# Kernel tuning notes

Measured on AMD Instinct MI355X. Metric: run time of the kernel, lower is better.

Reference implementation:

```python
import math
import jax, jax.numpy as jnp
import numpy as np

D_MODEL = 512
NUM_HEADS = 8
D_TRACK = 64
EPS = 1e-6


def setup_inputs() -> dict:
    key = jax.random.key(0)
    ks = jax.random.split(key, 8)
    B, C, T = 2, 4096, 16
    lecun = lambda k, shp: jax.random.normal(k, shp, jnp.float32) / jnp.sqrt(jnp.float32(shp[0]))
    return {
        "x": jax.random.normal(ks[0], (B, C, D_MODEL), jnp.float32),
        "track_embeddings": jax.random.normal(ks[1], (B, T, C, D_TRACK), jnp.float32),
        "norm_scale": jnp.ones((D_MODEL,), jnp.float32),
        "wq": lecun(ks[2], (D_MODEL, D_MODEL)), "bq": jnp.zeros((D_MODEL,), jnp.float32),
        "wk": lecun(ks[3], (D_TRACK, D_MODEL)), "bk": jnp.zeros((D_MODEL,), jnp.float32),
        "wv": lecun(ks[4], (D_TRACK, D_MODEL)), "bv": jnp.zeros((D_MODEL,), jnp.float32),
        "wo": lecun(ks[5], (D_MODEL, D_MODEL)), "bo": jnp.zeros((D_MODEL,), jnp.float32),
    }


def reference(x, track_embeddings, norm_scale, wq, bq, wk, bk, wv, bv, wo, bo):
    B, C, D = x.shape
    T = track_embeddings.shape[1]
    H = NUM_HEADS
    d_head = D // H
    residual = x
    # RMSNorm
    xn = x * jax.lax.rsqrt(jnp.mean(jnp.square(x), axis=-1, keepdims=True) + EPS) * norm_scale
    Q = (xn @ wq + bq).reshape(B, C, H, d_head)
    track_flat = track_embeddings.transpose(0, 2, 1, 3)  # (B, C, T, d_track)
    K = (track_flat @ wk + bk).reshape(B, C, T, H, d_head)
    V = (track_flat @ wv + bv).reshape(B, C, T, H, d_head)
    scale = 1.0 / math.sqrt(d_head)
    attn_logits = jnp.einsum('bchd,bcthd->bcht', Q, K) * scale
    attn_weights = jax.nn.softmax(attn_logits, axis=-1)
    attn_out = jnp.einsum('bcht,bcthd->bchd', attn_weights, V).reshape(B, C, D)
    return residual + attn_out @ wo + bo
```

## Files before the change

kernel.cpp:

```cpp
#include <hip/hip_runtime.h>
#include <math.h>


#define NTOK 8192

typedef __attribute__((ext_vector_type(8))) short short8;
typedef __attribute__((ext_vector_type(8))) unsigned short ushort8;
typedef __attribute__((ext_vector_type(4))) unsigned short ushort4v;
typedef __attribute__((ext_vector_type(4))) float f32x4;

__device__ __forceinline__ unsigned short f2bf(float f) {
    unsigned int u = __float_as_uint(f);
    unsigned int r = (u + 0x7fffu + ((u >> 16) & 1u)) >> 16;
    return (unsigned short)r;
}
__device__ __forceinline__ float bf2f(unsigned short s) {
    return __uint_as_float(((unsigned int)s) << 16);
}

__device__ __forceinline__ void gl_lds16(const void* g, void* l) {
    __builtin_amdgcn_global_load_lds(
        (const __attribute__((address_space(1))) unsigned int*)g,
        (__attribute__((address_space(3))) unsigned int*)l,
        16, 0, 0);
}


__global__ __launch_bounds__(256) void kprep(
    const float* __restrict__ x, const float* __restrict__ nscale,
    const float* __restrict__ wq, const float* __restrict__ bq,
    const float* __restrict__ wk, const float* __restrict__ wv,
    const float* __restrict__ bv, const float* __restrict__ wo,
    const float* __restrict__ bo,
    unsigned short* __restrict__ wqkT, float* __restrict__ bqk,
    unsigned short* __restrict__ wvoT, float* __restrict__ bvo,
    unsigned short* __restrict__ xnb)
{
    const int bid = blockIdx.x;
    const int t = threadIdx.x;
    if (bid < 64) {
        __shared__ float wkL[64][65];
        __shared__ float wqL[64][65];
        const int h = bid >> 3;
        const int i0 = (bid & 7) * 64;
        #pragma unroll
        for (int i = 0; i < 16; ++i) {
            const int idx = t + i * 256;
            const int d = idx >> 6, e = idx & 63;
            wkL[d][e] = wk[(size_t)d * 512 + h * 64 + e];
            wqL[d][e] = wq[(size_t)(i0 + d) * 512 + h * 64 + e];
        }
        __syncthreads();
        const int d = t & 63, ig = t >> 6;
        float acc[16];
        #pragma unroll
        for (int ii = 0; ii < 16; ++ii) acc[ii] = 0.f;
        for (int e = 0; e < 64; ++e) {
            const float kv = wkL[d][e];
            #pragma unroll
            for (int ii = 0; ii < 16; ++ii)
                acc[ii] += kv * wqL[ig * 16 + ii][e];
        }
        #pragma unroll
        for (int ii = 0; ii < 16; ++ii)
            wqkT[(size_t)(h * 64 + d) * 512 + i0 + ig * 16 + ii] = f2bf(acc[ii]);
        if (((bid & 7) == 0) && ig == 0) {
            float a = 0.f;
            #pragma unroll
            for (int e = 0; e < 64; ++e) a += bq[h * 64 + e] * wkL[d][e];
            bqk[h * 64 + d] = a;
        }
    } else if (bid < 128) {
        __shared__ float wvL[64][65];
        __shared__ float woL[64][65];
        const int b2 = bid - 64;
        const int h = b2 >> 3;
        const int j0 = (b2 & 7) * 64;
        #pragma unroll
        for (int i = 0; i < 16; ++i) {
            const int idx = t + i * 256;
            const int a = idx >> 6, b = idx & 63;
            wvL[a][b] = wv[(size_t)a * 512 + h * 64 + b];
            woL[a][b] = wo[(size_t)(h * 64 + a) * 512 + j0 + b];
        }
        __syncthreads();
        const int jloc = t & 63, dg = t >> 6;
        float acc[16];
        #pragma unroll
        for (int dd = 0; dd < 16; ++dd) acc[dd] = 0.f;
        for (int e = 0; e < 64; ++e) {
            const float b = woL[e][jloc];
            #pragma unroll
            for (int dd = 0; dd < 16; ++dd)
                acc[dd] += wvL[dg * 16 + dd][e] * b;
        }
        #pragma unroll
        for (int dd = 0; dd < 16; ++dd)
            wvoT[(size_t)(j0 + jloc) * 512 + h * 64 + dg * 16 + dd] = f2bf(acc[dd]);
    } else if (bid < 192) {
        const int b3 = bid - 128;
        const int j = b3 * 8 + (t >> 5);
        const int l = t & 31;
        float p = 0.f;
        #pragma unroll 4
        for (int e = l; e < 512; e += 32) p += bv[e] * wo[(size_t)e * 512 + j];
        #pragma unroll
        for (int m = 1; m < 32; m <<= 1) p += __shfl_xor(p, m, 64);
        if (l == 0) bvo[j] = bo[j] + p;
    } else {
        const int row = (bid - 192) * 4 + (t >> 6);
        const int lane = t & 63;
        const float* xr = x + (size_t)row * 512 + lane * 8;
        const float4 v0 = *reinterpret_cast<const float4*>(xr);
        const float4 v1 = *reinterpret_cast<const float4*>(xr + 4);
        float s = v0.x*v0.x + v0.y*v0.y + v0.z*v0.z + v0.w*v0.w
                + v1.x*v1.x + v1.y*v1.y + v1.z*v1.z + v1.w*v1.w;
        #pragma unroll
        for (int m = 1; m < 64; m <<= 1) s += __shfl_xor(s, m, 64);
        const float r = rsqrtf(s * (1.f / 512.f) + 1e-6f);
        const float4 s0 = *reinterpret_cast<const float4*>(nscale + lane * 8);
        const float4 s1 = *reinterpret_cast<const float4*>(nscale + lane * 8 + 4);
        ushort8 o;
        o[0] = f2bf(v0.x * r * s0.x); o[1] = f2bf(v0.y * r * s0.y);
        o[2] = f2bf(v0.z * r * s0.z); o[3] = f2bf(v0.w * r * s0.w);
        o[4] = f2bf(v1.x * r * s1.x); o[5] = f2bf(v1.y * r * s1.y);
        o[6] = f2bf(v1.z * r * s1.z); o[7] = f2bf(v1.w * r * s1.w);
        *reinterpret_cast<ushort8*>(xnb + (size_t)row * 512 + lane * 8) = o;
    }
}


template<int MODE>
__global__ __launch_bounds__(256) void kG(
    const unsigned short* __restrict__ A,
    const unsigned short* __restrict__ Bt,
    const float* __restrict__ bias,
    const float* __restrict__ resid,
    void* __restrict__ outp)
{
    __shared__ __align__(16) unsigned short Asm[2][128 * 64];
    __shared__ __align__(16) unsigned short Bsm[2][64 * 64];
    const int tid = threadIdx.x;
    const int hw = blockIdx.x;
    const int logical = (hw & 7) * 64 + (hw >> 3);
    const int mt = logical >> 3, nt = logical & 7;
    const int tok0 = mt * 128, n0 = nt * 64;
    const int w = tid >> 6, lane = tid & 63;
    const int wr = w >> 1, wc = w & 1;
    const int lrow = lane & 15, lk = lane >> 4;

    float pb[2];
    float rr[2][4][4];
    #pragma unroll
    for (int n = 0; n < 2; ++n) {
        const int ocol = n0 + wc * 32 + n * 16 + lrow;
        pb[n] = bias[ocol];
        if (MODE == 1) {
            #pragma unroll
            for (int m = 0; m < 4; ++m)
                #pragma unroll
                for (int r = 0; r < 4; ++r) {
                    const int orow = tok0 + wr * 64 + m * 16 + lk * 4 + r;
                    rr[n][m][r] = resid[(size_t)orow * 512 + ocol];
                }
        }
    }

    const int srowA[4] = { (tid + 0) >> 3, (tid + 256) >> 3, (tid + 512) >> 3, (tid + 768) >> 3 };
    const int sc8 = tid & 7;

    auto STAGE = [&](int buf, int k0) {
        #pragma unroll
        for (int i = 0; i < 4; ++i) {
            const int f = tid + i * 256;
            const int row = srowA[i];
            const int c8s = sc8 ^ (row & 7);
            gl_lds16(A + (size_t)(tok0 + row) * 512 + k0 + c8s * 8,
                     (char*)&Asm[buf][0] + f * 16);
        }
        #pragma unroll
        for (int i = 0; i < 2; ++i) {
            const int f = tid + i * 256;
            const int row = f >> 3;
            const int c8s = sc8 ^ (row & 7);
            gl_lds16(Bt + (size_t)(n0 + row) * 512 + k0 + c8s * 8,
                     (char*)&Bsm[buf][0] + f * 16);
        }
    };

    f32x4 acc[4][2] = {};
    STAGE(0, 0);
    __syncthreads();
    for (int it = 0; it < 8; ++it) {
        const int cur = it & 1;
        if (it < 7) STAGE(cur ^ 1, (it + 1) * 64);
        #pragma unroll
        for (int kk = 0; kk < 2; ++kk) {
            short8 a[4], b[2];
            #pragma unroll
            for (int m = 0; m < 4; ++m) {
                const int r = wr * 64 + m * 16 + lrow;
                const int byte = (r * 128 + kk * 64 + lk * 16) ^ ((r & 7) << 4);
                a[m] = *reinterpret_cast<const short8*>((const char*)&Asm[cur][0] + byte);
            }
            #pragma unroll
            for (int n = 0; n < 2; ++n) {
                const int r = wc * 32 + n * 16 + lrow;
                const int byte = (r * 128 + kk * 64 + lk * 16) ^ ((r & 7) << 4);
                b[n] = *reinterpret_cast<const short8*>((const char*)&Bsm[cur][0] + byte);
            }
            #pragma unroll
            for (int m = 0; m < 4; ++m)
                #pragma unroll
                for (int n = 0; n < 2; ++n)
                    acc[m][n] = __builtin_amdgcn_mfma_f32_16x16x32_bf16(
                        a[m], b[n], acc[m][n], 0, 0, 0);
        }
        __syncthreads();
    }
    #pragma unroll
    for (int n = 0; n < 2; ++n) {
        const int ocol = n0 + wc * 32 + n * 16 + lrow;
        #pragma unroll
        for (int m = 0; m < 4; ++m) {
            #pragma unroll
            for (int r = 0; r < 4; ++r) {
                const int orow = tok0 + wr * 64 + m * 16 + lk * 4 + r;
                float v = acc[m][n][r] + pb[n];
                if (MODE == 0) {
                    ((unsigned short*)outp)[(size_t)orow * 512 + ocol] = f2bf(v);
                } else {
                    v += rr[n][m][r];
                    ((float*)outp)[(size_t)orow * 512 + ocol] = v;
                }
            }
        }
    }
}


__global__ __launch_bounds__(256) void k3_attn(
    const float* __restrict__ track, const unsigned short* __restrict__ qwb,
    unsigned short* __restrict__ wtfb)
{
    __shared__ __align__(16) float tf[2][16][68];
    __shared__ __align__(16) float qwl[2][8][68];
    __shared__ float lw[2][8][16];
    const int tid = threadIdx.x;
    const int tok = tid >> 7;
    const int t2 = tid & 127;
    const int token = blockIdx.x * 2 + tok;
    const int b = token >> 12;
    const int c = token & 4095;
    #pragma unroll
    for (int i = 0; i < 2; ++i) {
        const int f = t2 + i * 128;
        const int row = f >> 4, d4 = (f & 15) * 4;
        *reinterpret_cast<float4*>(&tf[tok][row][d4]) =
            *reinterpret_cast<const float4*>(track + ((size_t)(b * 16 + row) * 4096 + c) * 64 + d4);
    }
    if (t2 < 64) {
        const ushort8 q = *reinterpret_cast<const ushort8*>(qwb + (size_t)token * 512 + t2 * 8);
        #pragma unroll
        for (int j = 0; j < 8; ++j) {
            const int idx = t2 * 8 + j;
            qwl[tok][idx >> 6][idx & 63] = bf2f(q[j]);
        }
    }
    __syncthreads();
    {
        const int h = t2 >> 4, tt = t2 & 15;
        float acc = 0.f;
        #pragma unroll
        for (int d16 = 0; d16 < 16; ++d16) {
            const float4 qv = *reinterpret_cast<const float4*>(&qwl[tok][h][d16 * 4]);
            const float4 tv = *reinterpret_cast<const float4*>(&tf[tok][tt][d16 * 4]);
            acc += qv.x * tv.x + qv.y * tv.y + qv.z * tv.z + qv.w * tv.w;
        }
        float lg = acc * 0.125f;
        float mx = lg;
        #pragma unroll
        for (int m = 1; m < 16; m <<= 1) mx = fmaxf(mx, __shfl_xor(mx, m, 64));
        const float ev = __expf(lg - mx);
        float sum = ev;
        #pragma unroll
        for (int m = 1; m < 16; m <<= 1) sum += __shfl_xor(sum, m, 64);
        lw[tok][h][tt] = ev / sum;
    }
    __syncthreads();
    {
        const int h = t2 >> 4;
        const int d0 = (t2 & 15) * 4;
        float o0 = 0.f, o1 = 0.f, o2 = 0.f, o3 = 0.f;
        #pragma unroll
        for (int t = 0; t < 16; ++t) {
            const float wgt = lw[tok][h][t];
            const float4 tv = *reinterpret_cast<const float4*>(&tf[tok][t][d0]);
            o0 += wgt * tv.x; o1 += wgt * tv.y; o2 += wgt * tv.z; o3 += wgt * tv.w;
        }
        ushort4v ov;
        ov[0] = f2bf(o0); ov[1] = f2bf(o1); ov[2] = f2bf(o2); ov[3] = f2bf(o3);
        *reinterpret_cast<ushort4v*>(wtfb + (size_t)token * 512 + t2 * 4) = ov;
    }
}

extern "C" void kernel_launch(void* const* d_in, const int* in_sizes, int n_in,
                              void* d_out, int out_size, void* d_ws, size_t ws_size,
                              hipStream_t stream) {
    const float* x      = (const float*)d_in[0];
    const float* track  = (const float*)d_in[1];
    const float* nscale = (const float*)d_in[2];
    const float* wq     = (const float*)d_in[3];
    const float* bq     = (const float*)d_in[4];
    const float* wk     = (const float*)d_in[5];
    const float* wv     = (const float*)d_in[7];
    const float* bv     = (const float*)d_in[8];
    const float* wo     = (const float*)d_in[9];
    const float* bo     = (const float*)d_in[10];
    float* buf = (float*)d_out;

    char* ws = (char*)d_ws;
    unsigned short* xnb  = (unsigned short*)ws;
    unsigned short* qwb  = (unsigned short*)(ws + 8388608);
    unsigned short* wqkT = (unsigned short*)(ws + 16777216);
    unsigned short* wvoT = (unsigned short*)(ws + 17301504);
    float* bqk = (float*)(ws + 17825792);
    float* bvo = (float*)(ws + 17827840);

    kprep<<<192 + NTOK / 4, 256, 0, stream>>>(x, nscale, wq, bq, wk, wv, bv, wo, bo,
                                              wqkT, bqk, wvoT, bvo, xnb);
    kG<0><<<512, 256, 0, stream>>>(xnb, wqkT, bqk, nullptr, qwb);
    k3_attn<<<NTOK / 2, 256, 0, stream>>>(track, qwb, xnb);
    kG<1><<<512, 256, 0, stream>>>(xnb, wvoT, bvo, x, buf);
}
```

Baseline: 52.35 us.

## Fuse RMSNorm, Q·Wk projection and track attention into one kernel

Removes the separate RMSNorm pass and the bf16 xn/qw intermediates. The new kernel loads fp32 x directly, converts it to bf16 in LDS and accumulates the sum of squares on the fly. It folds norm_scale into the precomputed Wq·Wk weights and applies the rsqrt row scale after the MFMA GEMM. The per-head attention over the 16 track slots runs in the same block, staging the track data via async global-to-LDS loads. This cuts a kernel launch and several global round-trips. In exchange the attention phase now runs per 64-column head tile with 8 tokens per step, and track data is reloaded once per head tile.

Measured after the change: 79.81 us. 52.5% more time.

```diff
diff --git a/kernel.cpp b/kernel.cpp
--- a/kernel.cpp
+++ b/kernel.cpp
@@ -6,7 +6,7 @@
 
 typedef __attribute__((ext_vector_type(8))) short short8;
 typedef __attribute__((ext_vector_type(8))) unsigned short ushort8;
-typedef __attribute__((ext_vector_type(4))) unsigned short ushort4v;
+typedef __attribute__((ext_vector_type(2))) unsigned short ushort2v;
 typedef __attribute__((ext_vector_type(4))) float f32x4;
 
 __device__ __forceinline__ unsigned short f2bf(float f) {
@@ -17,7 +17,6 @@
 __device__ __forceinline__ float bf2f(unsigned short s) {
     return __uint_as_float(((unsigned int)s) << 16);
 }
-
 __device__ __forceinline__ void gl_lds16(const void* g, void* l) {
     __builtin_amdgcn_global_load_lds(
         (const __attribute__((address_space(1))) unsigned int*)g,
@@ -27,14 +26,12 @@
 
 
 __global__ __launch_bounds__(256) void kprep(
-    const float* __restrict__ x, const float* __restrict__ nscale,
     const float* __restrict__ wq, const float* __restrict__ bq,
     const float* __restrict__ wk, const float* __restrict__ wv,
     const float* __restrict__ bv, const float* __restrict__ wo,
-    const float* __restrict__ bo,
+    const float* __restrict__ bo, const float* __restrict__ nscale,
     unsigned short* __restrict__ wqkT, float* __restrict__ bqk,
-    unsigned short* __restrict__ wvoT, float* __restrict__ bvo,
-    unsigned short* __restrict__ xnb)
+    unsigned short* __restrict__ wvoT, float* __restrict__ bvo)
 {
     const int bid = blockIdx.x;
     const int t = threadIdx.x;
@@ -62,8 +59,10 @@
                 acc[ii] += kv * wqL[ig * 16 + ii][e];
         }
         #pragma unroll
-        for (int ii = 0; ii < 16; ++ii)
-            wqkT[(size_t)(h * 64 + d) * 512 + i0 + ig * 16 + ii] = f2bf(acc[ii]);
+        for (int ii = 0; ii < 16; ++ii) {
+            const int i = i0 + ig * 16 + ii;
+            wqkT[(size_t)(h * 64 + d) * 512 + i] = f2bf(acc[ii] * nscale[i]);
+        }
         if (((bid & 7) == 0) && ig == 0) {
             float a = 0.f;
             #pragma unroll
@@ -97,7 +96,7 @@
         #pragma unroll
         for (int dd = 0; dd < 16; ++dd)
             wvoT[(size_t)(j0 + jloc) * 512 + h * 64 + dg * 16 + dd] = f2bf(acc[dd]);
-    } else if (bid < 192) {
+    } else {
         const int b3 = bid - 128;
         const int j = b3 * 8 + (t >> 5);
         const int l = t & 31;
@@ -107,36 +106,195 @@
         #pragma unroll
         for (int m = 1; m < 32; m <<= 1) p += __shfl_xor(p, m, 64);
         if (l == 0) bvo[j] = bo[j] + p;
-    } else {
-        const int row = (bid - 192) * 4 + (t >> 6);
-        const int lane = t & 63;
-        const float* xr = x + (size_t)row * 512 + lane * 8;
-        const float4 v0 = *reinterpret_cast<const float4*>(xr);
-        const float4 v1 = *reinterpret_cast<const float4*>(xr + 4);
-        float s = v0.x*v0.x + v0.y*v0.y + v0.z*v0.z + v0.w*v0.w
-                + v1.x*v1.x + v1.y*v1.y + v1.z*v1.z + v1.w*v1.w;
-        #pragma unroll
-        for (int m = 1; m < 64; m <<= 1) s += __shfl_xor(s, m, 64);
-        const float r = rsqrtf(s * (1.f / 512.f) + 1e-6f);
-        const float4 s0 = *reinterpret_cast<const float4*>(nscale + lane * 8);
-        const float4 s1 = *reinterpret_cast<const float4*>(nscale + lane * 8 + 4);
-        ushort8 o;
-        o[0] = f2bf(v0.x * r * s0.x); o[1] = f2bf(v0.y * r * s0.y);
-        o[2] = f2bf(v0.z * r * s0.z); o[3] = f2bf(v0.w * r * s0.w);
-        o[4] = f2bf(v1.x * r * s1.x); o[5] = f2bf(v1.y * r * s1.y);
-        o[6] = f2bf(v1.z * r * s1.z); o[7] = f2bf(v1.w * r * s1.w);
-        *reinterpret_cast<ushort8*>(xnb + (size_t)row * 512 + lane * 8) = o;
-    }
-}
-
-
-template<int MODE>
-__global__ __launch_bounds__(256) void kG(
+    }
+}
+
+
+__global__ __launch_bounds__(256) void kF(
+    const float* __restrict__ x, const float* __restrict__ track,
+    const unsigned short* __restrict__ wqkT, const float* __restrict__ bqk,
+    unsigned short* __restrict__ wtfb)
+{
+    __shared__ __align__(16) char pool[81920];
+    const int tid = threadIdx.x;
+    const int hw = blockIdx.x;
+    const int logical = (hw & 7) * 64 + (hw >> 3);
+    const int mt = logical >> 3, nt = logical & 7;
+    const int tok0 = mt * 128, n0 = nt * 64;
+    const int w = tid >> 6, lane = tid & 63;
+    const int wr = w >> 1, wc = w & 1;
+    const int lrow = lane & 15, lk = lane >> 4;
+    float* rls = (float*)(pool + 49152);
+
+    float pb[2];
+    #pragma unroll
+    for (int n = 0; n < 2; ++n) pb[n] = bqk[n0 + wc * 32 + n * 16 + lrow];
+
+    const int arow = tid >> 1;
+    const int ac0 = (tid & 1) * 4;
+    const float* xrow = x + (size_t)(tok0 + arow) * 512 + ac0 * 8;
+
+    auto stageB = [&](int buf, int k0) {
+        #pragma unroll
+        for (int i = 0; i < 2; ++i) {
+            const int f = tid + i * 256;
+            const int row = f >> 3, c8 = f & 7;
+            const int c8s = c8 ^ (row & 7);
+            gl_lds16(wqkT + (size_t)(n0 + row) * 512 + k0 + c8s * 8,
+                     pool + 32768 + buf * 8192 + f * 16);
+        }
+    };
+
+    float ssq = 0.f;
+    float4 v[8];
+    auto packA = [&](int buf) {
+        #pragma unroll
+        for (int c2 = 0; c2 < 4; ++c2) {
+            const float4 a0 = v[c2 * 2], a1 = v[c2 * 2 + 1];
+            ssq += a0.x*a0.x + a0.y*a0.y + a0.z*a0.z + a0.w*a0.w
+                 + a1.x*a1.x + a1.y*a1.y + a1.z*a1.z + a1.w*a1.w;
+            ushort8 o;
+            o[0]=f2bf(a0.x); o[1]=f2bf(a0.y); o[2]=f2bf(a0.z); o[3]=f2bf(a0.w);
+            o[4]=f2bf(a1.x); o[5]=f2bf(a1.y); o[6]=f2bf(a1.z); o[7]=f2bf(a1.w);
+            *reinterpret_cast<ushort8*>(
+                pool + buf * 16384 + arow * 128 + (((ac0 + c2) ^ (arow & 7)) << 4)) = o;
+        }
+    };
+
+    #pragma unroll
+    for (int j = 0; j < 8; ++j) v[j] = *reinterpret_cast<const float4*>(xrow + j * 4);
+    stageB(0, 0);
+    packA(0);
+    __syncthreads();
+
+    f32x4 acc[4][2] = {};
+    for (int it = 0; it < 8; ++it) {
+        const int cur = it & 1;
+        if (it < 7) {
+            stageB(cur ^ 1, (it + 1) * 64);
+            #pragma unroll
+            for (int j = 0; j < 8; ++j)
+                v[j] = *reinterpret_cast<const float4*>(xrow + (it + 1) * 64 + j * 4);
+        }
+        #pragma unroll
+        for (int kk = 0; kk < 2; ++kk) {
+            short8 a[4], b[2];
+            #pragma unroll
+            for (int m = 0; m < 4; ++m) {
+                const int r = wr * 64 + m * 16 + lrow;
+                const int byte = (r * 128 + kk * 64 + lk * 16) ^ ((r & 7) << 4);
+                a[m] = *reinterpret_cast<const short8*>(pool + cur * 16384 + byte);
+            }
+            #pragma unroll
+            for (int n = 0; n < 2; ++n) {
+                const int rB = wc * 32 + n * 16 + lrow;
+                const int byte = (rB * 128 + kk * 64 + lk * 16) ^ ((rB & 7) << 4);
+                b[n] = *reinterpret_cast<const short8*>(pool + 32768 + cur * 8192 + byte);
+            }
+            #pragma unroll
+            for (int m = 0; m < 4; ++m)
+                #pragma unroll
+                for (int n = 0; n < 2; ++n)
+                    acc[m][n] = __builtin_amdgcn_mfma_f32_16x16x32_bf16(
+                        a[m], b[n], acc[m][n], 0, 0, 0);
+        }
+        if (it < 7) packA(cur ^ 1);
+        __syncthreads();
+    }
+
+    {
+        const float tot = ssq + __shfl_xor(ssq, 1, 64);
+        if ((tid & 1) == 0) rls[arow] = rsqrtf(tot * (1.f / 512.f) + 1e-6f);
+    }
+    __syncthreads();
+
+    auto stageTF = [&](int pbuf, int p) {
+        char* base = pool + 16384 + pbuf * 32768;
+        #pragma unroll
+        for (int i = 0; i < 8; ++i) {
+            const int f = tid + i * 256;
+            const int tl = f >> 8, t = (f >> 4) & 15, dc = f & 15;
+            const int token = tok0 + p * 8 + tl;
+            const int bb = token >> 12, cc = token & 4095;
+            const int dcs = dc ^ (t & 7);
+            gl_lds16(track + ((size_t)(bb * 16 + t) * 4096 + cc) * 64 + dcs * 4,
+                     base + f * 16);
+        }
+    };
+    stageTF(0, 0);
+
+    #pragma unroll
+    for (int n = 0; n < 2; ++n) {
+        const int col = wc * 32 + n * 16 + lrow;
+        #pragma unroll
+        for (int m = 0; m < 4; ++m) {
+            #pragma unroll
+            for (int r2 = 0; r2 < 4; ++r2) {
+                const int row = wr * 64 + m * 16 + lk * 4 + r2;
+                const float qv = acc[m][n][r2] * rls[row] + pb[n];
+                *reinterpret_cast<unsigned short*>(
+                    pool + row * 128 + (((col >> 3) ^ (row & 7)) << 4) + (col & 7) * 2) = f2bf(qv);
+            }
+        }
+    }
+    __syncthreads();
+
+    const int tl = tid >> 5;
+    const int sub = tid & 31;
+    const int tslot = sub & 15, half = sub >> 4;
+    const int dpv = sub * 2;
+    for (int p = 0; p < 16; ++p) {
+        if (p < 15) stageTF((p + 1) & 1, p + 1);
+        const char* TFb = pool + 16384 + (p & 1) * 32768;
+        const char* tokb = TFb + tl * 4096;
+        const int qrow = p * 8 + tl;
+        float qf[32];
+        #pragma unroll
+        for (int jq = 0; jq < 4; ++jq) {
+            const ushort8 qv = *reinterpret_cast<const ushort8*>(
+                pool + qrow * 128 + (((half * 4 + jq) ^ (qrow & 7)) << 4));
+            #pragma unroll
+            for (int e = 0; e < 8; ++e) qf[jq * 8 + e] = bf2f((unsigned short)qv[e]);
+        }
+        float acc1 = 0.f;
+        #pragma unroll
+        for (int jj = 0; jj < 8; ++jj) {
+            const float4 tv = *reinterpret_cast<const float4*>(
+                tokb + tslot * 256 + (((half * 8 + jj) ^ (tslot & 7)) << 4));
+            acc1 += qf[jj*4+0]*tv.x + qf[jj*4+1]*tv.y + qf[jj*4+2]*tv.z + qf[jj*4+3]*tv.w;
+        }
+        acc1 += __shfl_xor(acc1, 16, 64);
+        const float lg = acc1 * 0.125f;
+        float mx = lg;
+        #pragma unroll
+        for (int msk = 1; msk < 16; msk <<= 1) mx = fmaxf(mx, __shfl_xor(mx, msk, 64));
+        const float ev = __expf(lg - mx);
+        float sm = ev;
+        #pragma unroll
+        for (int msk = 1; msk < 16; msk <<= 1) sm += __shfl_xor(sm, msk, 64);
+        const float wgt = ev / sm;
+        float o0 = 0.f, o1 = 0.f;
+        #pragma unroll
+        for (int t = 0; t < 16; ++t) {
+            const float wt = __shfl(wgt, (lane & 48) + t, 64);
+            const float2 tv = *reinterpret_cast<const float2*>(
+                tokb + t * 256 + (((dpv >> 2) ^ (t & 7)) << 4) + (dpv & 3) * 4);
+            o0 += wt * tv.x; o1 += wt * tv.y;
+        }
+        ushort2v ow; ow[0] = f2bf(o0); ow[1] = f2bf(o1);
+        const int token = tok0 + p * 8 + tl;
+        *reinterpret_cast<ushort2v*>(wtfb + (size_t)token * 512 + n0 + dpv) = ow;
+        __syncthreads();
+    }
+}
+
+
+__global__ __launch_bounds__(256) void kG2(
     const unsigned short* __restrict__ A,
     const unsigned short* __restrict__ Bt,
     const float* __restrict__ bias,
     const float* __restrict__ resid,
-    void* __restrict__ outp)
+    float* __restrict__ out)
 {
     __shared__ __align__(16) unsigned short Asm[2][128 * 64];
     __shared__ __align__(16) unsigned short Bsm[2][64 * 64];
@@ -155,20 +313,17 @@
     for (int n = 0; n < 2; ++n) {
         const int ocol = n0 + wc * 32 + n * 16 + lrow;
         pb[n] = bias[ocol];
-        if (MODE == 1) {
-            #pragma unroll
-            for (int m = 0; m < 4; ++m)
-                #pragma unroll
-                for (int r = 0; r < 4; ++r) {
-                    const int orow = tok0 + wr * 64 + m * 16 + lk * 4 + r;
-                    rr[n][m][r] = resid[(size_t)orow * 512 + ocol];
-                }
-        }
+        #pragma unroll
+        for (int m = 0; m < 4; ++m)
+            #pragma unroll
+            for (int r = 0; r < 4; ++r) {
+                const int orow = tok0 + wr * 64 + m * 16 + lk * 4 + r;
+                rr[n][m][r] = resid[(size_t)orow * 512 + ocol];
+            }
     }
 
     const int srowA[4] = { (tid + 0) >> 3, (tid + 256) >> 3, (tid + 512) >> 3, (tid + 768) >> 3 };
     const int sc8 = tid & 7;
-
     auto STAGE = [&](int buf, int k0) {
         #pragma unroll
         for (int i = 0; i < 4; ++i) {
@@ -226,81 +381,9 @@
             #pragma unroll
             for (int r = 0; r < 4; ++r) {
                 const int orow = tok0 + wr * 64 + m * 16 + lk * 4 + r;
-                float v = acc[m][n][r] + pb[n];
-                if (MODE == 0) {
-                    ((unsigned short*)outp)[(size_t)orow * 512 + ocol] = f2bf(v);
-                } else {
-                    v += rr[n][m][r];
-                    ((float*)outp)[(size_t)orow * 512 + ocol] = v;
-                }
-            }
-        }
-    }
-}
-
-
-__global__ __launch_bounds__(256) void k3_attn(
-    const float* __restrict__ track, const unsigned short* __restrict__ qwb,
-    unsigned short* __restrict__ wtfb)
-{
-    __shared__ __align__(16) float tf[2][16][68];
-    __shared__ __align__(16) float qwl[2][8][68];
-    __shared__ float lw[2][8][16];
-    const int tid = threadIdx.x;
-    const int tok = tid >> 7;
-    const int t2 = tid & 127;
-    const int token = blockIdx.x * 2 + tok;
-    const int b = token >> 12;
-    const int c = token & 4095;
-    #pragma unroll
-    for (int i = 0; i < 2; ++i) {
-        const int f = t2 + i * 128;
-        const int row = f >> 4, d4 = (f & 15) * 4;
-        *reinterpret_cast<float4*>(&tf[tok][row][d4]) =
-            *reinterpret_cast<const float4*>(track + ((size_t)(b * 16 + row) * 4096 + c) * 64 + d4);
-    }
-    if (t2 < 64) {
-        const ushort8 q = *reinterpret_cast<const ushort8*>(qwb + (size_t)token * 512 + t2 * 8);
-        #pragma unroll
-        for (int j = 0; j < 8; ++j) {
-            const int idx = t2 * 8 + j;
-            qwl[tok][idx >> 6][idx & 63] = bf2f(q[j]);
-        }
-    }
-    __syncthreads();
-    {
-        const int h = t2 >> 4, tt = t2 & 15;
-        float acc = 0.f;
-        #pragma unroll
-        for (int d16 = 0; d16 < 16; ++d16) {
-            const float4 qv = *reinterpret_cast<const float4*>(&qwl[tok][h][d16 * 4]);
-            const float4 tv = *reinterpret_cast<const float4*>(&tf[tok][tt][d16 * 4]);
-            acc += qv.x * tv.x + qv.y * tv.y + qv.z * tv.z + qv.w * tv.w;
-        }
-        float lg = acc * 0.125f;
-        float mx = lg;
-        #pragma unroll
-        for (int m = 1; m < 16; m <<= 1) mx = fmaxf(mx, __shfl_xor(mx, m, 64));
-        const float ev = __expf(lg - mx);
-        float sum = ev;
-        #pragma unroll
-        for (int m = 1; m < 16; m <<= 1) sum += __shfl_xor(sum, m, 64);
-        lw[tok][h][tt] = ev / sum;
-    }
-    __syncthreads();
-    {
-        const int h = t2 >> 4;
-        const int d0 = (t2 & 15) * 4;
-        float o0 = 0.f, o1 = 0.f, o2 = 0.f, o3 = 0.f;
-        #pragma unroll
-        for (int t = 0; t < 16; ++t) {
-            const float wgt = lw[tok][h][t];
-            const float4 tv = *reinterpret_cast<const float4*>(&tf[tok][t][d0]);
-            o0 += wgt * tv.x; o1 += wgt * tv.y; o2 += wgt * tv.z; o3 += wgt * tv.w;
-        }
-        ushort4v ov;
-        ov[0] = f2bf(o0); ov[1] = f2bf(o1); ov[2] = f2bf(o2); ov[3] = f2bf(o3);
-        *reinterpret_cast<ushort4v*>(wtfb + (size_t)token * 512 + t2 * 4) = ov;
+                out[(size_t)orow * 512 + ocol] = acc[m][n][r] + pb[n] + rr[n][m][r];
+            }
+        }
     }
 }
 
@@ -320,16 +403,14 @@
     float* buf = (float*)d_out;
 
     char* ws = (char*)d_ws;
-    unsigned short* xnb  = (unsigned short*)ws;
-    unsigned short* qwb  = (unsigned short*)(ws + 8388608);
-    unsigned short* wqkT = (unsigned short*)(ws + 16777216);
-    unsigned short* wvoT = (unsigned short*)(ws + 17301504);
-    float* bqk = (float*)(ws + 17825792);
-    float* bvo = (float*)(ws + 17827840);
-
-    kprep<<<192 + NTOK / 4, 256, 0, stream>>>(x, nscale, wq, bq, wk, wv, bv, wo, bo,
-                                              wqkT, bqk, wvoT, bvo, xnb);
-    kG<0><<<512, 256, 0, stream>>>(xnb, wqkT, bqk, nullptr, qwb);
-    k3_attn<<<NTOK / 2, 256, 0, stream>>>(track, qwb, xnb);
-    kG<1><<<512, 256, 0, stream>>>(xnb, wvoT, bvo, x, buf);
-}
+    unsigned short* wtfb = (unsigned short*)ws;
+    unsigned short* wqkT = (unsigned short*)(ws + 8388608);
+    unsigned short* wvoT = (unsigned short*)(ws + 8912896);
+    float* bqk = (float*)(ws + 9437184);
+    float* bvo = (float*)(ws + 9439232);
+
+    kprep<<<192, 256, 0, stream>>>(wq, bq, wk, wv, bv, wo, bo, nscale,
+                                   wqkT, bqk, wvoT, bvo);
+    kF<<<512, 256, 0, stream>>>(x, track, wqkT, bqk, wtfb);
+    kG2<<<512, 256, 0, stream>>>(wtfb, wvoT, bvo, x, buf);
+}
```

## Fuse RMSNorm into the Q·Wk GEMM and fold norm scale into weights

Applied to the files above, without the earlier changes.

RMSNorm moves out of the prep kernel and into the first GEMM. The GEMM loads fp32 x directly, converts it to bf16 into LDS while accumulating per-row sums of squares, and applies the rsqrt row scale in the epilogue. The norm scale is folded into the precomputed Wq·Wk^T weights, and the 1/sqrt(d) factor moves from the attention kernel into the GEMM epilogue. This removes the bf16 normalized-x round trip through global memory, at the cost of register-staged A loads in place of direct global-to-LDS copies and twice the A-tile read bytes, since the input is now fp32.

Measured after the change: 61.64 us. 17.7% more time.

```diff
diff --git a/kernel.cpp b/kernel.cpp
--- a/kernel.cpp
+++ b/kernel.cpp
@@ -17,7 +17,6 @@
 __device__ __forceinline__ float bf2f(unsigned short s) {
     return __uint_as_float(((unsigned int)s) << 16);
 }
-
 __device__ __forceinline__ void gl_lds16(const void* g, void* l) {
     __builtin_amdgcn_global_load_lds(
         (const __attribute__((address_space(1))) unsigned int*)g,
@@ -27,14 +26,12 @@
 
 
 __global__ __launch_bounds__(256) void kprep(
-    const float* __restrict__ x, const float* __restrict__ nscale,
     const float* __restrict__ wq, const float* __restrict__ bq,
     const float* __restrict__ wk, const float* __restrict__ wv,
     const float* __restrict__ bv, const float* __restrict__ wo,
-    const float* __restrict__ bo,
+    const float* __restrict__ bo, const float* __restrict__ nscale,
     unsigned short* __restrict__ wqkT, float* __restrict__ bqk,
-    unsigned short* __restrict__ wvoT, float* __restrict__ bvo,
-    unsigned short* __restrict__ xnb)
+    unsigned short* __restrict__ wvoT, float* __restrict__ bvo)
 {
     const int bid = blockIdx.x;
     const int t = threadIdx.x;
@@ -62,8 +59,10 @@
                 acc[ii] += kv * wqL[ig * 16 + ii][e];
         }
         #pragma unroll
-        for (int ii = 0; ii < 16; ++ii)
-            wqkT[(size_t)(h * 64 + d) * 512 + i0 + ig * 16 + ii] = f2bf(acc[ii]);
+        for (int ii = 0; ii < 16; ++ii) {
+            const int i = i0 + ig * 16 + ii;
+            wqkT[(size_t)(h * 64 + d) * 512 + i] = f2bf(acc[ii] * nscale[i]);
+        }
         if (((bid & 7) == 0) && ig == 0) {
             float a = 0.f;
             #pragma unroll
@@ -97,7 +96,7 @@
         #pragma unroll
         for (int dd = 0; dd < 16; ++dd)
             wvoT[(size_t)(j0 + jloc) * 512 + h * 64 + dg * 16 + dd] = f2bf(acc[dd]);
-    } else if (bid < 192) {
+    } else {
         const int b3 = bid - 128;
         const int j = b3 * 8 + (t >> 5);
         const int l = t & 31;
@@ -107,39 +106,18 @@
         #pragma unroll
         for (int m = 1; m < 32; m <<= 1) p += __shfl_xor(p, m, 64);
         if (l == 0) bvo[j] = bo[j] + p;
-    } else {
-        const int row = (bid - 192) * 4 + (t >> 6);
-        const int lane = t & 63;
-        const float* xr = x + (size_t)row * 512 + lane * 8;
-        const float4 v0 = *reinterpret_cast<const float4*>(xr);
-        const float4 v1 = *reinterpret_cast<const float4*>(xr + 4);
-        float s = v0.x*v0.x + v0.y*v0.y + v0.z*v0.z + v0.w*v0.w
-                + v1.x*v1.x + v1.y*v1.y + v1.z*v1.z + v1.w*v1.w;
-        #pragma unroll
-        for (int m = 1; m < 64; m <<= 1) s += __shfl_xor(s, m, 64);
-        const float r = rsqrtf(s * (1.f / 512.f) + 1e-6f);
-        const float4 s0 = *reinterpret_cast<const float4*>(nscale + lane * 8);
-        const float4 s1 = *reinterpret_cast<const float4*>(nscale + lane * 8 + 4);
-        ushort8 o;
-        o[0] = f2bf(v0.x * r * s0.x); o[1] = f2bf(v0.y * r * s0.y);
-        o[2] = f2bf(v0.z * r * s0.z); o[3] = f2bf(v0.w * r * s0.w);
-        o[4] = f2bf(v1.x * r * s1.x); o[5] = f2bf(v1.y * r * s1.y);
-        o[6] = f2bf(v1.z * r * s1.z); o[7] = f2bf(v1.w * r * s1.w);
-        *reinterpret_cast<ushort8*>(xnb + (size_t)row * 512 + lane * 8) = o;
-    }
-}
-
-
-template<int MODE>
-__global__ __launch_bounds__(256) void kG(
-    const unsigned short* __restrict__ A,
-    const unsigned short* __restrict__ Bt,
-    const float* __restrict__ bias,
-    const float* __restrict__ resid,
-    void* __restrict__ outp)
+    }
+}
+
+
+__global__ __launch_bounds__(256) void kRG1(
+    const float* __restrict__ x,
+    const unsigned short* __restrict__ wqkT, const float* __restrict__ bqk,
+    unsigned short* __restrict__ qwb)
 {
     __shared__ __align__(16) unsigned short Asm[2][128 * 64];
     __shared__ __align__(16) unsigned short Bsm[2][64 * 64];
+    __shared__ float rls[128];
     const int tid = threadIdx.x;
     const int hw = blockIdx.x;
     const int logical = (hw & 7) * 64 + (hw >> 3);
@@ -150,50 +128,62 @@
     const int lrow = lane & 15, lk = lane >> 4;
 
     float pb[2];
-    float rr[2][4][4];
-    #pragma unroll
-    for (int n = 0; n < 2; ++n) {
-        const int ocol = n0 + wc * 32 + n * 16 + lrow;
-        pb[n] = bias[ocol];
-        if (MODE == 1) {
-            #pragma unroll
-            for (int m = 0; m < 4; ++m)
-                #pragma unroll
-                for (int r = 0; r < 4; ++r) {
-                    const int orow = tok0 + wr * 64 + m * 16 + lk * 4 + r;
-                    rr[n][m][r] = resid[(size_t)orow * 512 + ocol];
-                }
-        }
-    }
-
-    const int srowA[4] = { (tid + 0) >> 3, (tid + 256) >> 3, (tid + 512) >> 3, (tid + 768) >> 3 };
+    #pragma unroll
+    for (int n = 0; n < 2; ++n) pb[n] = bqk[n0 + wc * 32 + n * 16 + lrow];
+
+    const int aj = tid >> 4, ac4 = tid & 15;
     const int sc8 = tid & 7;
 
-    auto STAGE = [&](int buf, int k0) {
-        #pragma unroll
-        for (int i = 0; i < 4; ++i) {
-            const int f = tid + i * 256;
-            const int row = srowA[i];
-            const int c8s = sc8 ^ (row & 7);
-            gl_lds16(A + (size_t)(tok0 + row) * 512 + k0 + c8s * 8,
-                     (char*)&Asm[buf][0] + f * 16);
-        }
+    auto stageB = [&](int buf, int k0) {
         #pragma unroll
         for (int i = 0; i < 2; ++i) {
             const int f = tid + i * 256;
-            const int row = f >> 3;
-            const int c8s = sc8 ^ (row & 7);
-            gl_lds16(Bt + (size_t)(n0 + row) * 512 + k0 + c8s * 8,
+            const int row = f >> 3, c8 = f & 7;
+            const int c8s = c8 ^ (row & 7);
+            gl_lds16(wqkT + (size_t)(n0 + row) * 512 + k0 + c8s * 8,
                      (char*)&Bsm[buf][0] + f * 16);
         }
     };
 
+    float ssq[8];
+    #pragma unroll
+    for (int i = 0; i < 8; ++i) ssq[i] = 0.f;
+    float4 v[8];
+
+    auto loadA = [&](int it) {
+        #pragma unroll
+        for (int i = 0; i < 8; ++i) {
+            const int row = aj + 16 * i;
+            v[i] = *reinterpret_cast<const float4*>(
+                x + (size_t)(tok0 + row) * 512 + it * 64 + ac4 * 4);
+        }
+    };
+    auto packA = [&](int buf) {
+        #pragma unroll
+        for (int i = 0; i < 8; ++i) {
+            const int row = aj + 16 * i;
+            ssq[i] += v[i].x*v[i].x + v[i].y*v[i].y + v[i].z*v[i].z + v[i].w*v[i].w;
+            ushort4v o;
+            o[0] = f2bf(v[i].x); o[1] = f2bf(v[i].y);
+            o[2] = f2bf(v[i].z); o[3] = f2bf(v[i].w);
+            *reinterpret_cast<ushort4v*>(
+                (char*)&Asm[buf][0] + row * 128 + (((ac4 >> 1) ^ (row & 7)) << 4)
+                + (ac4 & 1) * 8) = o;
+        }
+    };
+
+    stageB(0, 0);
+    loadA(0);
+    packA(0);
+    __syncthreads();
+
     f32x4 acc[4][2] = {};
-    STAGE(0, 0);
-    __syncthreads();
     for (int it = 0; it < 8; ++it) {
         const int cur = it & 1;
-        if (it < 7) STAGE(cur ^ 1, (it + 1) * 64);
+        if (it < 7) {
+            stageB(cur ^ 1, (it + 1) * 64);
+            loadA(it + 1);
+        }
         #pragma unroll
         for (int kk = 0; kk < 2; ++kk) {
             short8 a[4], b[2];
@@ -205,8 +195,8 @@
             }
             #pragma unroll
             for (int n = 0; n < 2; ++n) {
-                const int r = wc * 32 + n * 16 + lrow;
-                const int byte = (r * 128 + kk * 64 + lk * 16) ^ ((r & 7) << 4);
+                const int rB = wc * 32 + n * 16 + lrow;
+                const int byte = (rB * 128 + kk * 64 + lk * 16) ^ ((rB & 7) << 4);
                 b[n] = *reinterpret_cast<const short8*>((const char*)&Bsm[cur][0] + byte);
             }
             #pragma unroll
@@ -216,8 +206,22 @@
                     acc[m][n] = __builtin_amdgcn_mfma_f32_16x16x32_bf16(
                         a[m], b[n], acc[m][n], 0, 0, 0);
         }
+        if (it < 7) packA(cur ^ 1);
         __syncthreads();
     }
+
+    #pragma unroll
+    for (int i = 0; i < 8; ++i) {
+        #pragma unroll
+        for (int msk = 1; msk < 16; msk <<= 1) ssq[i] += __shfl_xor(ssq[i], msk, 64);
+    }
+    if ((tid & 15) == 0) {
+        #pragma unroll
+        for (int i = 0; i < 8; ++i)
+            rls[aj + 16 * i] = rsqrtf(ssq[i] * (1.f / 512.f) + 1e-6f);
+    }
+    __syncthreads();
+
     #pragma unroll
     for (int n = 0; n < 2; ++n) {
         const int ocol = n0 + wc * 32 + n * 16 + lrow;
@@ -225,14 +229,9 @@
         for (int m = 0; m < 4; ++m) {
             #pragma unroll
             for (int r = 0; r < 4; ++r) {
-                const int orow = tok0 + wr * 64 + m * 16 + lk * 4 + r;
-                float v = acc[m][n][r] + pb[n];
-                if (MODE == 0) {
-                    ((unsigned short*)outp)[(size_t)orow * 512 + ocol] = f2bf(v);
-                } else {
-                    v += rr[n][m][r];
-                    ((float*)outp)[(size_t)orow * 512 + ocol] = v;
-                }
+                const int row = wr * 64 + m * 16 + lk * 4 + r;
+                const float qv = (acc[m][n][r] * rls[row] + pb[n]) * 0.125f;
+                qwb[(size_t)(tok0 + row) * 512 + ocol] = f2bf(qv);
             }
         }
     }
@@ -277,7 +276,7 @@
             const float4 tv = *reinterpret_cast<const float4*>(&tf[tok][tt][d16 * 4]);
             acc += qv.x * tv.x + qv.y * tv.y + qv.z * tv.z + qv.w * tv.w;
         }
-        float lg = acc * 0.125f;
+        const float lg = acc;
         float mx = lg;
         #pragma unroll
         for (int m = 1; m < 16; m <<= 1) mx = fmaxf(mx, __shfl_xor(mx, m, 64));
@@ -301,6 +300,105 @@
         ushort4v ov;
         ov[0] = f2bf(o0); ov[1] = f2bf(o1); ov[2] = f2bf(o2); ov[3] = f2bf(o3);
         *reinterpret_cast<ushort4v*>(wtfb + (size_t)token * 512 + t2 * 4) = ov;
+    }
+}
+
+
+__global__ __launch_bounds__(256) void kG2(
+    const unsigned short* __restrict__ A,
+    const unsigned short* __restrict__ Bt,
+    const float* __restrict__ bias,
+    const float* __restrict__ resid,
+    float* __restrict__ out)
+{
+    __shared__ __align__(16) unsigned short Asm[2][128 * 64];
+    __shared__ __align__(16) unsigned short Bsm[2][64 * 64];
+    const int tid = threadIdx.x;
+    const int hw = blockIdx.x;
+    const int logical = (hw & 7) * 64 + (hw >> 3);
+    const int mt = logical >> 3, nt = logical & 7;
+    const int tok0 = mt * 128, n0 = nt * 64;
+    const int w = tid >> 6, lane = tid & 63;
+    const int wr = w >> 1, wc = w & 1;
+    const int lrow = lane & 15, lk = lane >> 4;
+
+    float pb[2];
+    float rr[2][4][4];
+    #pragma unroll
+    for (int n = 0; n < 2; ++n) {
+        const int ocol = n0 + wc * 32 + n * 16 + lrow;
+        pb[n] = bias[ocol];
+        #pragma unroll
+        for (int m = 0; m < 4; ++m)
+            #pragma unroll
+            for (int r = 0; r < 4; ++r) {
+                const int orow = tok0 + wr * 64 + m * 16 + lk * 4 + r;
+                rr[n][m][r] = resid[(size_t)orow * 512 + ocol];
+            }
+    }
+
+    const int srowA[4] = { (tid + 0) >> 3, (tid + 256) >> 3, (tid + 512) >> 3, (tid + 768) >> 3 };
+    const int sc8 = tid & 7;
+    auto STAGE = [&](int buf, int k0) {
+        #pragma unroll
+        for (int i = 0; i < 4; ++i) {
+            const int f = tid + i * 256;
+            const int row = srowA[i];
+            const int c8s = sc8 ^ (row & 7);
+            gl_lds16(A + (size_t)(tok0 + row) * 512 + k0 + c8s * 8,
+                     (char*)&Asm[buf][0] + f * 16);
+        }
+        #pragma unroll
+        for (int i = 0; i < 2; ++i) {
+            const int f = tid + i * 256;
+            const int row = f >> 3;
+            const int c8s = sc8 ^ (row & 7);
+            gl_lds16(Bt + (size_t)(n0 + row) * 512 + k0 + c8s * 8,
+                     (char*)&Bsm[buf][0] + f * 16);
+        }
+    };
+
+    f32x4 acc[4][2] = {};
+    STAGE(0, 0);
+    __syncthreads();
+    for (int it = 0; it < 8; ++it) {
+        const int cur = it & 1;
+        if (it < 7) STAGE(cur ^ 1, (it + 1) * 64);
+        #pragma unroll
+        for (int kk = 0; kk < 2; ++kk) {
+            short8 a[4], b[2];
+            #pragma unroll
+            for (int m = 0; m < 4; ++m) {
+                const int r = wr * 64 + m * 16 + lrow;
+                const int byte = (r * 128 + kk * 64 + lk * 16) ^ ((r & 7) << 4);
+                a[m] = *reinterpret_cast<const short8*>((const char*)&Asm[cur][0] + byte);
+            }
+            #pragma unroll
+            for (int n = 0; n < 2; ++n) {
+                const int r = wc * 32 + n * 16 + lrow;
+                const int byte = (r * 128 + kk * 64 + lk * 16) ^ ((r & 7) << 4);
+                b[n] = *reinterpret_cast<const short8*>((const char*)&Bsm[cur][0] + byte);
+            }
+            #pragma unroll
+            for (int m = 0; m < 4; ++m)
+                #pragma unroll
+                for (int n = 0; n < 2; ++n)
+                    acc[m][n] = __builtin_amdgcn_mfma_f32_16x16x32_bf16(
+                        a[m], b[n], acc[m][n], 0, 0, 0);
+        }
+        __syncthreads();
+    }
+    #pragma unroll
+    for (int n = 0; n < 2; ++n) {
+        const int ocol = n0 + wc * 32 + n * 16 + lrow;
+        #pragma unroll
+        for (int m = 0; m < 4; ++m) {
+            #pragma unroll
+            for (int r = 0; r < 4; ++r) {
+                const int orow = tok0 + wr * 64 + m * 16 + lk * 4 + r;
+                out[(size_t)orow * 512 + ocol] = acc[m][n][r] + pb[n] + rr[n][m][r];
+            }
+        }
     }
 }
 
@@ -320,16 +418,16 @@
     float* buf = (float*)d_out;
 
     char* ws = (char*)d_ws;
-    unsigned short* xnb  = (unsigned short*)ws;
-    unsigned short* qwb  = (unsigned short*)(ws + 8388608);
+    unsigned short* qwb  = (unsigned short*)ws;
+    unsigned short* wtfb = (unsigned short*)(ws + 8388608);
     unsigned short* wqkT = (unsigned short*)(ws + 16777216);
     unsigned short* wvoT = (unsigned short*)(ws + 17301504);
     float* bqk = (float*)(ws + 17825792);
     float* bvo = (float*)(ws + 17827840);
 
-    kprep<<<192 + NTOK / 4, 256, 0, stream>>>(x, nscale, wq, bq, wk, wv, bv, wo, bo,
-                                              wqkT, bqk, wvoT, bvo, xnb);
-    kG<0><<<512, 256, 0, stream>>>(xnb, wqkT, bqk, nullptr, qwb);
-    k3_attn<<<NTOK / 2, 256, 0, stream>>>(track, qwb, xnb);
-    kG<1><<<512, 256, 0, stream>>>(xnb, wvoT, bvo, x, buf);
-}
+    kprep<<<192, 256, 0, stream>>>(wq, bq, wk, wv, bv, wo, bo, nscale,
+                                   wqkT, bqk, wvoT, bvo);
+    kRG1<<<512, 256, 0, stream>>>(x, wqkT, bqk, qwb);
+    k3_attn<<<NTOK / 2, 256, 0, stream>>>(track, qwb, wtfb);
+    kG2<<<512, 256, 0, stream>>>(wtfb, wvoT, bvo, x, buf);
+}
```

## Fuse Q-projection GEMM with per-head track attention into one kernel

Applied to the files above, without the earlier changes.

Folds the attention step into the epilogue of the Q·Wk GEMM. Each 128x64 output tile (one head, 128 tokens) is written to LDS as scaled bf16, and each wave then streams the track rows for its 32 tokens through double-buffered async global-to-LDS loads to compute softmax and the weighted sum. This removes the separate attention kernel and the bf16 round trip of the 8192x512 Q intermediate through global memory. In exchange, each block reloads the track embeddings per head (8x redundant track reads across n-tiles), and the attention loop is serialized per token within each wave.

After: 74.76 us. +42.8%, slower.

```diff
diff --git a/kernel.cpp b/kernel.cpp
--- a/kernel.cpp
+++ b/kernel.cpp
@@ -17,7 +17,6 @@
 __device__ __forceinline__ float bf2f(unsigned short s) {
     return __uint_as_float(((unsigned int)s) << 16);
 }
-
 __device__ __forceinline__ void gl_lds16(const void* g, void* l) {
     __builtin_amdgcn_global_load_lds(
         (const __attribute__((address_space(1))) unsigned int*)g,
@@ -130,13 +129,166 @@
 }
 
 
-template<int MODE>
-__global__ __launch_bounds__(256) void kG(
+__global__ __launch_bounds__(256) void kFA(
+    const unsigned short* __restrict__ A,
+    const unsigned short* __restrict__ Bt,
+    const float* __restrict__ bqk,
+    const float* __restrict__ track,
+    unsigned short* __restrict__ wtfb)
+{
+    __shared__ __align__(16) char pool[53248];
+    const int tid = threadIdx.x;
+    const int hw = blockIdx.x;
+    const int logical = (hw & 7) * 64 + (hw >> 3);
+    const int mt = logical >> 3, nt = logical & 7;
+    const int tok0 = mt * 128, n0 = nt * 64;
+    const int w = tid >> 6, lane = tid & 63;
+    const int wr = w >> 1, wc = w & 1;
+    const int lrow = lane & 15, lk = lane >> 4;
+
+    float pb[2];
+    #pragma unroll
+    for (int n = 0; n < 2; ++n) pb[n] = bqk[n0 + wc * 32 + n * 16 + lrow];
+
+    const int srowA[4] = { (tid + 0) >> 3, (tid + 256) >> 3, (tid + 512) >> 3, (tid + 768) >> 3 };
+    const int sc8 = tid & 7;
+    auto STAGE = [&](int buf, int k0) {
+        #pragma unroll
+        for (int i = 0; i < 4; ++i) {
+            const int f = tid + i * 256;
+            const int row = srowA[i];
+            const int c8s = sc8 ^ (row & 7);
+            gl_lds16(A + (size_t)(tok0 + row) * 512 + k0 + c8s * 8,
+                     pool + buf * 16384 + f * 16);
+        }
+        #pragma unroll
+        for (int i = 0; i < 2; ++i) {
+            const int f = tid + i * 256;
+            const int row = f >> 3;
+            const int c8s = sc8 ^ (row & 7);
+            gl_lds16(Bt + (size_t)(n0 + row) * 512 + k0 + c8s * 8,
+                     pool + 32768 + buf * 8192 + f * 16);
+        }
+    };
+
+    f32x4 acc[4][2] = {};
+    STAGE(0, 0);
+    __syncthreads();
+    for (int it = 0; it < 8; ++it) {
+        const int cur = it & 1;
+        if (it < 7) STAGE(cur ^ 1, (it + 1) * 64);
+        #pragma unroll
+        for (int kk = 0; kk < 2; ++kk) {
+            short8 a[4], b[2];
+            #pragma unroll
+            for (int m = 0; m < 4; ++m) {
+                const int r = wr * 64 + m * 16 + lrow;
+                const int byte = (r * 128 + kk * 64 + lk * 16) ^ ((r & 7) << 4);
+                a[m] = *reinterpret_cast<const short8*>(pool + cur * 16384 + byte);
+            }
+            #pragma unroll
+            for (int n = 0; n < 2; ++n) {
+                const int r = wc * 32 + n * 16 + lrow;
+                const int byte = (r * 128 + kk * 64 + lk * 16) ^ ((r & 7) << 4);
+                b[n] = *reinterpret_cast<const short8*>(pool + 32768 + cur * 8192 + byte);
+            }
+            #pragma unroll
+            for (int m = 0; m < 4; ++m)
+                #pragma unroll
+                for (int n = 0; n < 2; ++n)
+                    acc[m][n] = __builtin_amdgcn_mfma_f32_16x16x32_bf16(
+                        a[m], b[n], acc[m][n], 0, 0, 0);
+        }
+        __syncthreads();
+    }
+
+    char* TFw = pool + 20480 + w * 8192;
+    auto issueTF = [&](int b, int tokloc) {
+        const int token = tok0 + tokloc;
+        const int bb = token >> 12, cc = token & 4095;
+        char* base = TFw + b * 4096;
+        #pragma unroll
+        for (int q = 0; q < 4; ++q) {
+            const int f = lane + q * 64;
+            const int t = f >> 4, ch = f & 15;
+            const int chs = ch ^ (t & 7);
+            gl_lds16(track + ((size_t)(bb * 16 + t) * 4096 + cc) * 64 + chs * 4,
+                     base + f * 16);
+        }
+    };
+    issueTF(0, w * 32);
+
+    #pragma unroll
+    for (int n = 0; n < 2; ++n) {
+        const int col = wc * 32 + n * 16 + lrow;
+        #pragma unroll
+        for (int m = 0; m < 4; ++m) {
+            #pragma unroll
+            for (int r2 = 0; r2 < 4; ++r2) {
+                const int row = wr * 64 + m * 16 + lk * 4 + r2;
+                *reinterpret_cast<unsigned short*>(pool + row * 160 + col * 2) =
+                    f2bf((acc[m][n][r2] + pb[n]) * 0.125f);
+            }
+        }
+    }
+    __syncthreads();
+
+    const int tp = lane & 15, rep = lane >> 4;
+    const int pvch = lane >> 2, pvsub = lane & 3;
+    for (int i = 0; i < 32; ++i) {
+        if (i < 31) {
+            issueTF((i + 1) & 1, w * 32 + i + 1);
+            asm volatile("s_waitcnt vmcnt(4)" ::: "memory");
+        } else {
+            asm volatile("s_waitcnt vmcnt(0)" ::: "memory");
+        }
+        __builtin_amdgcn_sched_barrier(0);
+        const char* tb = TFw + (i & 1) * 4096;
+        const int row = w * 32 + i;
+        float qf[16];
+        #pragma unroll
+        for (int jq = 0; jq < 2; ++jq) {
+            const ushort8 qv = *reinterpret_cast<const ushort8*>(
+                pool + row * 160 + (rep * 2 + jq) * 16);
+            #pragma unroll
+            for (int e = 0; e < 8; ++e) qf[jq * 8 + e] = bf2f((unsigned short)qv[e]);
+        }
+        float a1 = 0.f;
+        #pragma unroll
+        for (int qq = 0; qq < 4; ++qq) {
+            const float4 tv = *reinterpret_cast<const float4*>(
+                tb + tp * 256 + (((rep * 4 + qq) ^ (tp & 7)) << 4));
+            a1 += qf[qq*4+0]*tv.x + qf[qq*4+1]*tv.y + qf[qq*4+2]*tv.z + qf[qq*4+3]*tv.w;
+        }
+        a1 += __shfl_xor(a1, 16, 64);
+        a1 += __shfl_xor(a1, 32, 64);
+        float mx = a1;
+        #pragma unroll
+        for (int msk = 1; msk < 16; msk <<= 1) mx = fmaxf(mx, __shfl_xor(mx, msk, 64));
+        const float ev = __expf(a1 - mx);
+        float sm = ev;
+        #pragma unroll
+        for (int msk = 1; msk < 16; msk <<= 1) sm += __shfl_xor(sm, msk, 64);
+        const float pw = ev / sm;
+        float o = 0.f;
+        #pragma unroll
+        for (int t = 0; t < 16; ++t) {
+            const float wt = __shfl(pw, t, 64);
+            const float tv = *reinterpret_cast<const float*>(
+                tb + t * 256 + ((pvch ^ (t & 7)) << 4) + pvsub * 4);
+            o += wt * tv;
+        }
+        wtfb[(size_t)(tok0 + row) * 512 + n0 + lane] = f2bf(o);
+    }
+}
+
+
+__global__ __launch_bounds__(256) void kG2(
     const unsigned short* __restrict__ A,
     const unsigned short* __restrict__ Bt,
     const float* __restrict__ bias,
     const float* __restrict__ resid,
-    void* __restrict__ outp)
+    float* __restrict__ out)
 {
     __shared__ __align__(16) unsigned short Asm[2][128 * 64];
     __shared__ __align__(16) unsigned short Bsm[2][64 * 64];
@@ -155,20 +307,17 @@
     for (int n = 0; n < 2; ++n) {
         const int ocol = n0 + wc * 32 + n * 16 + lrow;
         pb[n] = bias[ocol];
-        if (MODE == 1) {
-            #pragma unroll
-            for (int m = 0; m < 4; ++m)
-                #pragma unroll
-                for (int r = 0; r < 4; ++r) {
-                    const int orow = tok0 + wr * 64 + m * 16 + lk * 4 + r;
-                    rr[n][m][r] = resid[(size_t)orow * 512 + ocol];
-                }
-        }
+        #pragma unroll
+        for (int m = 0; m < 4; ++m)
+            #pragma unroll
+            for (int r = 0; r < 4; ++r) {
+                const int orow = tok0 + wr * 64 + m * 16 + lk * 4 + r;
+                rr[n][m][r] = resid[(size_t)orow * 512 + ocol];
+            }
     }
 
     const int srowA[4] = { (tid + 0) >> 3, (tid + 256) >> 3, (tid + 512) >> 3, (tid + 768) >> 3 };
     const int sc8 = tid & 7;
-
     auto STAGE = [&](int buf, int k0) {
         #pragma unroll
         for (int i = 0; i < 4; ++i) {
@@ -226,81 +375,9 @@
             #pragma unroll
             for (int r = 0; r < 4; ++r) {
                 const int orow = tok0 + wr * 64 + m * 16 + lk * 4 + r;
-                float v = acc[m][n][r] + pb[n];
-                if (MODE == 0) {
-                    ((unsigned short*)outp)[(size_t)orow * 512 + ocol] = f2bf(v);
-                } else {
-                    v += rr[n][m][r];
-                    ((float*)outp)[(size_t)orow * 512 + ocol] = v;
-                }
-            }
-        }
-    }
-}
-
-
-__global__ __launch_bounds__(256) void k3_attn(
-    const float* __restrict__ track, const unsigned short* __restrict__ qwb,
-    unsigned short* __restrict__ wtfb)
-{
-    __shared__ __align__(16) float tf[2][16][68];
-    __shared__ __align__(16) float qwl[2][8][68];
-    __shared__ float lw[2][8][16];
-    const int tid = threadIdx.x;
-    const int tok = tid >> 7;
-    const int t2 = tid & 127;
-    const int token = blockIdx.x * 2 + tok;
-    const int b = token >> 12;
-    const int c = token & 4095;
-    #pragma unroll
-    for (int i = 0; i < 2; ++i) {
-        const int f = t2 + i * 128;
-        const int row = f >> 4, d4 = (f & 15) * 4;
-        *reinterpret_cast<float4*>(&tf[tok][row][d4]) =
-            *reinterpret_cast<const float4*>(track + ((size_t)(b * 16 + row) * 4096 + c) * 64 + d4);
-    }
-    if (t2 < 64) {
-        const ushort8 q = *reinterpret_cast<const ushort8*>(qwb + (size_t)token * 512 + t2 * 8);
-        #pragma unroll
-        for (int j = 0; j < 8; ++j) {
-            const int idx = t2 * 8 + j;
-            qwl[tok][idx >> 6][idx & 63] = bf2f(q[j]);
-        }
-    }
-    __syncthreads();
-    {
-        const int h = t2 >> 4, tt = t2 & 15;
-        float acc = 0.f;
-        #pragma unroll
-        for (int d16 = 0; d16 < 16; ++d16) {
-            const float4 qv = *reinterpret_cast<const float4*>(&qwl[tok][h][d16 * 4]);
-            const float4 tv = *reinterpret_cast<const float4*>(&tf[tok][tt][d16 * 4]);
-            acc += qv.x * tv.x + qv.y * tv.y + qv.z * tv.z + qv.w * tv.w;
-        }
-        float lg = acc * 0.125f;
-        float mx = lg;
-        #pragma unroll
-        for (int m = 1; m < 16; m <<= 1) mx = fmaxf(mx, __shfl_xor(mx, m, 64));
-        const float ev = __expf(lg - mx);
-        float sum = ev;
-        #pragma unroll
-        for (int m = 1; m < 16; m <<= 1) sum += __shfl_xor(sum, m, 64);
-        lw[tok][h][tt] = ev / sum;
-    }
-    __syncthreads();
-    {
-        const int h = t2 >> 4;
-        const int d0 = (t2 & 15) * 4;
-        float o0 = 0.f, o1 = 0.f, o2 = 0.f, o3 = 0.f;
-        #pragma unroll
-        for (int t = 0; t < 16; ++t) {
-            const float wgt = lw[tok][h][t];
-            const float4 tv = *reinterpret_cast<const float4*>(&tf[tok][t][d0]);
-            o0 += wgt * tv.x; o1 += wgt * tv.y; o2 += wgt * tv.z; o3 += wgt * tv.w;
-        }
-        ushort4v ov;
-        ov[0] = f2bf(o0); ov[1] = f2bf(o1); ov[2] = f2bf(o2); ov[3] = f2bf(o3);
-        *reinterpret_cast<ushort4v*>(wtfb + (size_t)token * 512 + t2 * 4) = ov;
+                out[(size_t)orow * 512 + ocol] = acc[m][n][r] + pb[n] + rr[n][m][r];
+            }
+        }
     }
 }
 
@@ -321,7 +398,7 @@
 
     char* ws = (char*)d_ws;
     unsigned short* xnb  = (unsigned short*)ws;
-    unsigned short* qwb  = (unsigned short*)(ws + 8388608);
+    unsigned short* wtfb = (unsigned short*)(ws + 8388608);
     unsigned short* wqkT = (unsigned short*)(ws + 16777216);
     unsigned short* wvoT = (unsigned short*)(ws + 17301504);
     float* bqk = (float*)(ws + 17825792);
@@ -329,7 +406,6 @@
 
     kprep<<<192 + NTOK / 4, 256, 0, stream>>>(x, nscale, wq, bq, wk, wv, bv, wo, bo,
                                               wqkT, bqk, wvoT, bvo, xnb);
-    kG<0><<<512, 256, 0, stream>>>(xnb, wqkT, bqk, nullptr, qwb);
-    k3_attn<<<NTOK / 2, 256, 0, stream>>>(track, qwb, xnb);
-    kG<1><<<512, 256, 0, stream>>>(xnb, wvoT, bvo, x, buf);
-}
+    kFA<<<512, 256, 0, stream>>>(xnb, wqkT, bqk, track, wtfb);
+    kG2<<<512, 256, 0, stream>>>(wtfb, wvoT, bvo, x, buf);
+}
```
